# Performance work log

Hardware: AMD Instinct MI355X
Metric: run time of the kernel (lower is better)

## Reference

```python
import jax, jax.numpy as jnp
import numpy as np

N_CLUSTERS = 512
TEMPERATURE = 0.1


def setup_inputs() -> dict:
    key = jax.random.key(0)
    k1, k2 = jax.random.split(key)
    x = jax.random.normal(k1, (32, 1024, 256), dtype=jnp.float32)
    centroids = jax.random.normal(k2, (N_CLUSTERS, 256), dtype=jnp.float32)
    return {"x": x, "centroids": centroids}


def reference(x, centroids):
    # Flatten non-cluster axes into a sample axis: [N, D]
    B, S, D = x.shape
    xf = x.reshape(-1, D)  # [N, D]
    x_sq = jnp.sum(xf * xf, axis=-1, keepdims=True)           # [N, 1]
    c_sq = jnp.sum(centroids * centroids, axis=-1)             # [K]
    cross = jnp.einsum('nd,kd->nk', xf, centroids)             # [N, K]
    dists = x_sq - 2.0 * cross + c_sq[None, :]                 # [N, K]
    # Temperature-scaled soft assignments
    assignments = jax.nn.softmax(-dists / TEMPERATURE, axis=-1)  # [N, K]
    # Restore leading (non-feature) dims, append cluster axis
    return assignments.reshape(B, S, N_CLUSTERS)
```

## Files before the change

### kernel.cpp

```cpp
#include <hip/hip_runtime.h>

#define NROWS 32768
#define KC 512
#define DDIM 256
#define BM 128
#define BK 32
#define KCH (DDIM / BK)
#define CHUNK_USH (KC * BK)

typedef __attribute__((ext_vector_type(8))) short bf16x8;
typedef __attribute__((ext_vector_type(4))) float f32x4;

union U8 { unsigned short u[8]; bf16x8 v; };

__device__ __forceinline__ unsigned short f2bf(float f) {
    union { float f; unsigned int u; } a; a.f = f;
    unsigned int r = a.u + 0x7fffu + ((a.u >> 16) & 1u);
    return (unsigned short)(r >> 16);
}
__device__ __forceinline__ float bf2f(unsigned short h) {
    union { unsigned int u; float f; } a; a.u = ((unsigned int)h) << 16;
    return a.f;
}
__device__ __forceinline__ void ld16(const void* g, void* l) {
    __builtin_amdgcn_global_load_lds(
        (const __attribute__((address_space(1))) unsigned int*)g,
        (__attribute__((address_space(3))) unsigned int*)l, 16, 0, 0);
}

__global__ __launch_bounds__(64) void prep_c(const float* __restrict__ c,
                                             unsigned short* __restrict__ bhi,
                                             unsigned short* __restrict__ blo,
                                             float* __restrict__ csq10) {
    const int n = blockIdx.x, lane = threadIdx.x;
    const int d0 = lane * 4;
    float4 v = ((const float4*)(c + (size_t)n * DDIM))[lane];
    float vv[4] = {v.x, v.y, v.z, v.w};
    unsigned short hh[4], ll[4];
    float ssq = 0.f;
    #pragma unroll
    for (int i = 0; i < 4; ++i) {
        ssq += vv[i] * vv[i];
        hh[i] = f2bf(vv[i]);
        ll[i] = f2bf(vv[i] - bf2f(hh[i]));
    }
    #pragma unroll
    for (int off = 32; off; off >>= 1) ssq += __shfl_xor(ssq, off);
    if (lane == 0) csq10[n] = 10.f * ssq;
    const int ks = d0 >> 5;
    const int q  = (d0 >> 3) & 3;
    const int s  = q ^ ((n >> 1) & 3);
    const size_t dst = (size_t)ks * CHUNK_USH + (n * 4 + s) * 8 + (d0 & 7);
    *(ushort4*)(bhi + dst) = make_ushort4(hh[0], hh[1], hh[2], hh[3]);
    *(ushort4*)(blo + dst) = make_ushort4(ll[0], ll[1], ll[2], ll[3]);
}

union SmemU {
    struct { unsigned short Bh[2][CHUNK_USH], Bl[2][CHUNK_USH]; } k;
    float lbuf[32 * 516];
};

__global__ __launch_bounds__(512, 2) void kmeans_mfma(
    const float* __restrict__ x, const unsigned short* __restrict__ bhi,
    const unsigned short* __restrict__ blo, const float* __restrict__ csq10,
    float* __restrict__ out) {
    __shared__ __align__(16) SmemU sm;
    __shared__ float red[2][2][BM];

    const int tid  = threadIdx.x;
    const int w    = tid >> 6, lane = tid & 63;
    const int wm   = w >> 1, wn = w & 1;
    const int cc   = lane & 15, q = lane >> 4;
    const int row0 = blockIdx.x * BM;

    f32x4 acc[2][16];
    #pragma unroll
    for (int mt = 0; mt < 2; ++mt)
        #pragma unroll
        for (int t = 0; t < 16; ++t) acc[mt][t] = (f32x4){0.f, 0.f, 0.f, 0.f};

    const float* xA0 = x + (size_t)(row0 + wm * 32 + cc) * DDIM + q * 8;
    const float* xA1 = xA0 + (size_t)16 * DDIM;
    const int sF = q ^ ((cc >> 1) & 3);
    const int bF = (4 * cc + sF) * 8;
    const int dmaOff = (w * 4) * 512;

    #pragma unroll
    for (int j = 0; j < 4; ++j) {
        const int o = dmaOff + j * 512;
        ld16(bhi + o + lane * 8, &sm.k.Bh[0][o]);
        ld16(blo + o + lane * 8, &sm.k.Bl[0][o]);
    }
    float4 c00 = *(const float4*)xA0;
    float4 c01 = *(const float4*)(xA0 + 4);
    float4 c10 = *(const float4*)xA1;
    float4 c11 = *(const float4*)(xA1 + 4);
    __syncthreads();

    for (int ks = 0; ks < KCH; ++ks) {
        const int pp = ks & 1;
        float4 n00, n01, n10, n11;
        if (ks < KCH - 1) {
            const size_t cb = (size_t)(ks + 1) * CHUNK_USH;
            #pragma unroll
            for (int j = 0; j < 4; ++j) {
                const int o = dmaOff + j * 512;
                ld16(bhi + cb + o + lane * 8, &sm.k.Bh[1 - pp][o]);
                ld16(blo + cb + o + lane * 8, &sm.k.Bl[1 - pp][o]);
            }
            const int kn = (ks + 1) * BK;
            n00 = *(const float4*)(xA0 + kn);
            n01 = *(const float4*)(xA0 + kn + 4);
            n10 = *(const float4*)(xA1 + kn);
            n11 = *(const float4*)(xA1 + kn + 4);
        }
        bf16x8 ah[2], al[2];
        {
            float v0[8] = {c00.x, c00.y, c00.z, c00.w, c01.x, c01.y, c01.z, c01.w};
            float v1[8] = {c10.x, c10.y, c10.z, c10.w, c11.x, c11.y, c11.z, c11.w};
            U8 H0, L0, H1, L1;
            #pragma unroll
            for (int i = 0; i < 8; ++i) {
                H0.u[i] = f2bf(v0[i]); L0.u[i] = f2bf(v0[i] - bf2f(H0.u[i]));
                H1.u[i] = f2bf(v1[i]); L1.u[i] = f2bf(v1[i] - bf2f(H1.u[i]));
            }
            ah[0] = H0.v; al[0] = L0.v; ah[1] = H1.v; al[1] = L1.v;
        }
        #pragma unroll
        for (int t = 0; t < 16; ++t) {
            const int bo = (wn * 16 + t) * 512 + bF;
            bf16x8 bh = *(const bf16x8*)&sm.k.Bh[pp][bo];
            bf16x8 bl = *(const bf16x8*)&sm.k.Bl[pp][bo];
            acc[0][t] = __builtin_amdgcn_mfma_f32_16x16x32_bf16(ah[0], bh, acc[0][t], 0, 0, 0);
            acc[1][t] = __builtin_amdgcn_mfma_f32_16x16x32_bf16(ah[1], bh, acc[1][t], 0, 0, 0);
            acc[0][t] = __builtin_amdgcn_mfma_f32_16x16x32_bf16(ah[0], bl, acc[0][t], 0, 0, 0);
            acc[1][t] = __builtin_amdgcn_mfma_f32_16x16x32_bf16(ah[1], bl, acc[1][t], 0, 0, 0);
            acc[0][t] = __builtin_amdgcn_mfma_f32_16x16x32_bf16(al[0], bh, acc[0][t], 0, 0, 0);
            acc[1][t] = __builtin_amdgcn_mfma_f32_16x16x32_bf16(al[1], bh, acc[1][t], 0, 0, 0);
        }
        c00 = n00; c01 = n01; c10 = n10; c11 = n11;
        __syncthreads();
    }

    float csqv[16];
    #pragma unroll
    for (int t = 0; t < 16; ++t) csqv[t] = csq10[wn * 256 + t * 16 + cc];
    const int rb = wm * 32 + q * 4;
    float M[2][4], I[2][4];
    #pragma unroll
    for (int mt = 0; mt < 2; ++mt)
        #pragma unroll
        for (int g = 0; g < 4; ++g) {
            float pm = -1e30f;
            #pragma unroll
            for (int t = 0; t < 16; ++t) pm = fmaxf(pm, 20.f * acc[mt][t][g] - csqv[t]);
            #pragma unroll
            for (int off = 1; off < 16; off <<= 1) pm = fmaxf(pm, __shfl_xor(pm, off));
            if (cc == 0) red[0][wn][rb + mt * 16 + g] = pm;
            M[mt][g] = pm;
        }
    __syncthreads();
    #pragma unroll
    for (int mt = 0; mt < 2; ++mt)
        #pragma unroll
        for (int g = 0; g < 4; ++g) {
            M[mt][g] = fmaxf(M[mt][g], red[0][1 - wn][rb + mt * 16 + g]);
            float ps = 0.f;
            #pragma unroll
            for (int t = 0; t < 16; ++t) ps += __expf(20.f * acc[mt][t][g] - csqv[t] - M[mt][g]);
            #pragma unroll
            for (int off = 1; off < 16; off <<= 1) ps += __shfl_xor(ps, off);
            if (cc == 0) red[1][wn][rb + mt * 16 + g] = ps;
        }
    __syncthreads();
    #pragma unroll
    for (int mt = 0; mt < 2; ++mt)
        #pragma unroll
        for (int g = 0; g < 4; ++g)
            I[mt][g] = 1.f / (red[1][0][rb + mt * 16 + g] + red[1][1][rb + mt * 16 + g]);

    #pragma unroll
    for (int p = 0; p < 4; ++p) {
        if (wm == p) {
            #pragma unroll
            for (int mt = 0; mt < 2; ++mt)
                #pragma unroll
                for (int g = 0; g < 4; ++g) {
                    const int   lr = mt * 16 + q * 4 + g;
                    const float mg = M[mt][g], ig = I[mt][g];
                    #pragma unroll
                    for (int t = 0; t < 16; ++t)
                        sm.lbuf[lr * 516 + wn * 256 + t * 16 + cc] =
                            __expf(20.f * acc[mt][t][g] - csqv[t] - mg) * ig;
                }
        }
        __syncthreads();
        #pragma unroll
        for (int j = 0; j < 8; ++j) {
            const int f    = j * 512 + tid;
            const int lrow = f >> 7;
            const int c4   = f & 127;
            float4    v    = *(const float4*)&sm.lbuf[lrow * 516 + c4 * 4];
            *(float4*)(out + (size_t)(row0 + p * 32 + lrow) * KC + c4 * 4) = v;
        }
        __syncthreads();
    }
}

extern "C" void kernel_launch(void* const* d_in, const int* in_sizes, int n_in,
                              void* d_out, int out_size, void* d_ws, size_t ws_size,
                              hipStream_t stream) {
    const float* x   = (const float*)d_in[0];
    const float* c   = (const float*)d_in[1];
    float*       out = (float*)d_out;

    unsigned short* bhi   = (unsigned short*)d_ws;
    unsigned short* blo   = bhi + (size_t)KCH * CHUNK_USH;
    float*          csq10 = (float*)(blo + (size_t)KCH * CHUNK_USH);

    prep_c<<<KC, 64, 0, stream>>>(c, bhi, blo, csq10);
    kmeans_mfma<<<NROWS / BM, 512, 0, stream>>>(x, bhi, blo, csq10, out);
}
```

Before: 118.0 us.

## Halve row tile, single-buffer centroid smem, raise occupancy, stagger K start

Shrinks the row tile from 128 to 64 with a 2x4 warp grid, so each warp keeps 8 instead of 16 accumulator tiles. The centroid chunks move from double buffering to a single buffer, and launch bounds rise to 4 blocks per CU. This trades the overlap of loads with MFMA for more resident blocks and doubles the grid. Blocks also start at a staggered K-chunk offset, which is meant to spread L2 accesses to the centroid data, and the softmax reductions now combine four column warps.

Measured after the change: 122.8 us. 1.04x slower.

```diff
diff --git a/kernel.cpp b/kernel.cpp
--- a/kernel.cpp
+++ b/kernel.cpp
@@ -3,7 +3,7 @@
 #define NROWS 32768
 #define KC 512
 #define DDIM 256
-#define BM 128
+#define BM 64
 #define BK 32
 #define KCH (DDIM / BK)
 #define CHUNK_USH (KC * BK)
@@ -56,59 +56,58 @@
 }
 
 union SmemU {
-    struct { unsigned short Bh[2][CHUNK_USH], Bl[2][CHUNK_USH]; } k;
-    float lbuf[32 * 516];
+    struct { unsigned short Bh[CHUNK_USH], Bl[CHUNK_USH]; } k;
+    float lbuf[16 * 516];
 };
 
-__global__ __launch_bounds__(512, 2) void kmeans_mfma(
+__global__ __launch_bounds__(512, 4) void kmeans_mfma(
     const float* __restrict__ x, const unsigned short* __restrict__ bhi,
     const unsigned short* __restrict__ blo, const float* __restrict__ csq10,
     float* __restrict__ out) {
     __shared__ __align__(16) SmemU sm;
-    __shared__ float red[2][2][BM];
+    __shared__ float red[2][4][BM];
 
     const int tid  = threadIdx.x;
     const int w    = tid >> 6, lane = tid & 63;
-    const int wm   = w >> 1, wn = w & 1;
+    const int wm   = w >> 2, wn = w & 3;
     const int cc   = lane & 15, q = lane >> 4;
     const int row0 = blockIdx.x * BM;
 
-    f32x4 acc[2][16];
-    #pragma unroll
-    for (int mt = 0; mt < 2; ++mt)
-        #pragma unroll
-        for (int t = 0; t < 16; ++t) acc[mt][t] = (f32x4){0.f, 0.f, 0.f, 0.f};
+    f32x4 acc[2][8];
+    #pragma unroll
+    for (int mt = 0; mt < 2; ++mt)
+        #pragma unroll
+        for (int t = 0; t < 8; ++t) acc[mt][t] = (f32x4){0.f, 0.f, 0.f, 0.f};
 
     const float* xA0 = x + (size_t)(row0 + wm * 32 + cc) * DDIM + q * 8;
     const float* xA1 = xA0 + (size_t)16 * DDIM;
     const int sF = q ^ ((cc >> 1) & 3);
     const int bF = (4 * cc + sF) * 8;
-    const int dmaOff = (w * 4) * 512;
-
-    #pragma unroll
-    for (int j = 0; j < 4; ++j) {
-        const int o = dmaOff + j * 512;
-        ld16(bhi + o + lane * 8, &sm.k.Bh[0][o]);
-        ld16(blo + o + lane * 8, &sm.k.Bl[0][o]);
-    }
-    float4 c00 = *(const float4*)xA0;
-    float4 c01 = *(const float4*)(xA0 + 4);
-    float4 c10 = *(const float4*)xA1;
-    float4 c11 = *(const float4*)(xA1 + 4);
+    const int dmaOff = w * 2048;
+
+    const int s0 = ((blockIdx.x >> 3) & 1) * 4;
+
+    {
+        const size_t cb = (size_t)s0 * CHUNK_USH;
+        #pragma unroll
+        for (int j = 0; j < 4; ++j) {
+            const int o = dmaOff + j * 512;
+            ld16(bhi + cb + o + lane * 8, &sm.k.Bh[o]);
+            ld16(blo + cb + o + lane * 8, &sm.k.Bl[o]);
+        }
+    }
+    const int k0 = s0 * BK;
+    float4 c00 = *(const float4*)(xA0 + k0);
+    float4 c01 = *(const float4*)(xA0 + k0 + 4);
+    float4 c10 = *(const float4*)(xA1 + k0);
+    float4 c11 = *(const float4*)(xA1 + k0 + 4);
     __syncthreads();
 
-    for (int ks = 0; ks < KCH; ++ks) {
-        const int pp = ks & 1;
+    for (int i = 0; i < KCH; ++i) {
+        const int nks = (s0 + i + 1) & (KCH - 1);
         float4 n00, n01, n10, n11;
-        if (ks < KCH - 1) {
-            const size_t cb = (size_t)(ks + 1) * CHUNK_USH;
-            #pragma unroll
-            for (int j = 0; j < 4; ++j) {
-                const int o = dmaOff + j * 512;
-                ld16(bhi + cb + o + lane * 8, &sm.k.Bh[1 - pp][o]);
-                ld16(blo + cb + o + lane * 8, &sm.k.Bl[1 - pp][o]);
-            }
-            const int kn = (ks + 1) * BK;
+        if (i < KCH - 1) {
+            const int kn = nks * BK;
             n00 = *(const float4*)(xA0 + kn);
             n01 = *(const float4*)(xA0 + kn + 4);
             n10 = *(const float4*)(xA1 + kn);
@@ -120,17 +119,17 @@
             float v1[8] = {c10.x, c10.y, c10.z, c10.w, c11.x, c11.y, c11.z, c11.w};
             U8 H0, L0, H1, L1;
             #pragma unroll
-            for (int i = 0; i < 8; ++i) {
-                H0.u[i] = f2bf(v0[i]); L0.u[i] = f2bf(v0[i] - bf2f(H0.u[i]));
-                H1.u[i] = f2bf(v1[i]); L1.u[i] = f2bf(v1[i] - bf2f(H1.u[i]));
+            for (int e = 0; e < 8; ++e) {
+                H0.u[e] = f2bf(v0[e]); L0.u[e] = f2bf(v0[e] - bf2f(H0.u[e]));
+                H1.u[e] = f2bf(v1[e]); L1.u[e] = f2bf(v1[e] - bf2f(H1.u[e]));
             }
             ah[0] = H0.v; al[0] = L0.v; ah[1] = H1.v; al[1] = L1.v;
         }
         #pragma unroll
-        for (int t = 0; t < 16; ++t) {
-            const int bo = (wn * 16 + t) * 512 + bF;
-            bf16x8 bh = *(const bf16x8*)&sm.k.Bh[pp][bo];
-            bf16x8 bl = *(const bf16x8*)&sm.k.Bl[pp][bo];
+        for (int t = 0; t < 8; ++t) {
+            const int bo = (wn * 8 + t) * 512 + bF;
+            bf16x8 bh = *(const bf16x8*)&sm.k.Bh[bo];
+            bf16x8 bl = *(const bf16x8*)&sm.k.Bl[bo];
             acc[0][t] = __builtin_amdgcn_mfma_f32_16x16x32_bf16(ah[0], bh, acc[0][t], 0, 0, 0);
             acc[1][t] = __builtin_amdgcn_mfma_f32_16x16x32_bf16(ah[1], bh, acc[1][t], 0, 0, 0);
             acc[0][t] = __builtin_amdgcn_mfma_f32_16x16x32_bf16(ah[0], bl, acc[0][t], 0, 0, 0);
@@ -138,13 +137,23 @@
             acc[0][t] = __builtin_amdgcn_mfma_f32_16x16x32_bf16(al[0], bh, acc[0][t], 0, 0, 0);
             acc[1][t] = __builtin_amdgcn_mfma_f32_16x16x32_bf16(al[1], bh, acc[1][t], 0, 0, 0);
         }
+        __syncthreads();
+        if (i < KCH - 1) {
+            const size_t cb = (size_t)nks * CHUNK_USH;
+            #pragma unroll
+            for (int j = 0; j < 4; ++j) {
+                const int o = dmaOff + j * 512;
+                ld16(bhi + cb + o + lane * 8, &sm.k.Bh[o]);
+                ld16(blo + cb + o + lane * 8, &sm.k.Bl[o]);
+            }
+            __syncthreads();
+        }
         c00 = n00; c01 = n01; c10 = n10; c11 = n11;
-        __syncthreads();
-    }
-
-    float csqv[16];
-    #pragma unroll
-    for (int t = 0; t < 16; ++t) csqv[t] = csq10[wn * 256 + t * 16 + cc];
+    }
+
+    float csqv[8];
+    #pragma unroll
+    for (int t = 0; t < 8; ++t) csqv[t] = csq10[wn * 128 + t * 16 + cc];
     const int rb = wm * 32 + q * 4;
     float M[2][4], I[2][4];
     #pragma unroll
@@ -153,55 +162,59 @@
         for (int g = 0; g < 4; ++g) {
             float pm = -1e30f;
             #pragma unroll
-            for (int t = 0; t < 16; ++t) pm = fmaxf(pm, 20.f * acc[mt][t][g] - csqv[t]);
+            for (int t = 0; t < 8; ++t) pm = fmaxf(pm, 20.f * acc[mt][t][g] - csqv[t]);
             #pragma unroll
             for (int off = 1; off < 16; off <<= 1) pm = fmaxf(pm, __shfl_xor(pm, off));
             if (cc == 0) red[0][wn][rb + mt * 16 + g] = pm;
-            M[mt][g] = pm;
         }
     __syncthreads();
     #pragma unroll
     for (int mt = 0; mt < 2; ++mt)
         #pragma unroll
         for (int g = 0; g < 4; ++g) {
-            M[mt][g] = fmaxf(M[mt][g], red[0][1 - wn][rb + mt * 16 + g]);
+            const int ri = rb + mt * 16 + g;
+            const float m = fmaxf(fmaxf(red[0][0][ri], red[0][1][ri]),
+                                  fmaxf(red[0][2][ri], red[0][3][ri]));
+            M[mt][g] = m;
             float ps = 0.f;
             #pragma unroll
-            for (int t = 0; t < 16; ++t) ps += __expf(20.f * acc[mt][t][g] - csqv[t] - M[mt][g]);
+            for (int t = 0; t < 8; ++t) ps += __expf(20.f * acc[mt][t][g] - csqv[t] - m);
             #pragma unroll
             for (int off = 1; off < 16; off <<= 1) ps += __shfl_xor(ps, off);
-            if (cc == 0) red[1][wn][rb + mt * 16 + g] = ps;
+            if (cc == 0) red[1][wn][ri] = ps;
         }
     __syncthreads();
     #pragma unroll
     for (int mt = 0; mt < 2; ++mt)
         #pragma unroll
-        for (int g = 0; g < 4; ++g)
-            I[mt][g] = 1.f / (red[1][0][rb + mt * 16 + g] + red[1][1][rb + mt * 16 + g]);
+        for (int g = 0; g < 4; ++g) {
+            const int ri = rb + mt * 16 + g;
+            I[mt][g] = 1.f / (red[1][0][ri] + red[1][1][ri] +
+                              red[1][2][ri] + red[1][3][ri]);
+        }
 
     #pragma unroll
     for (int p = 0; p < 4; ++p) {
-        if (wm == p) {
-            #pragma unroll
-            for (int mt = 0; mt < 2; ++mt)
+        if (wm == (p >> 1)) {
+            const int mt = p & 1;
+            #pragma unroll
+            for (int g = 0; g < 4; ++g) {
+                const int   lr = q * 4 + g;
+                const float mg = M[mt][g], ig = I[mt][g];
                 #pragma unroll
-                for (int g = 0; g < 4; ++g) {
-                    const int   lr = mt * 16 + q * 4 + g;
-                    const float mg = M[mt][g], ig = I[mt][g];
-                    #pragma unroll
-                    for (int t = 0; t < 16; ++t)
-                        sm.lbuf[lr * 516 + wn * 256 + t * 16 + cc] =
-                            __expf(20.f * acc[mt][t][g] - csqv[t] - mg) * ig;
-                }
+                for (int t = 0; t < 8; ++t)
+                    sm.lbuf[lr * 516 + wn * 128 + t * 16 + cc] =
+                        __expf(20.f * acc[mt][t][g] - csqv[t] - mg) * ig;
+            }
         }
         __syncthreads();
         #pragma unroll
-        for (int j = 0; j < 8; ++j) {
+        for (int j = 0; j < 4; ++j) {
             const int f    = j * 512 + tid;
             const int lrow = f >> 7;
             const int c4   = f & 127;
             float4    v    = *(const float4*)&sm.lbuf[lrow * 516 + c4 * 4];
-            *(float4*)(out + (size_t)(row0 + p * 32 + lrow) * KC + c4 * 4) = v;
+            *(float4*)(out + (size_t)(row0 + p * 16 + lrow) * KC + c4 * 4) = v;
         }
         __syncthreads();
     }
```

## Load centroid fragments directly from global into registers, drop LDS staging

Applied to the files above, without the earlier changes.

Rewrites prep_c so the bf16 hi/lo centroid fragments are stored in a lane-contiguous MFMA fragment order. The main kernel then loads them straight from global memory into registers, double-buffered two tiles ahead, instead of DMA-staging them through LDS. This removes the LDS ping-pong buffers and the per-chunk __syncthreads, which should also cut LDS use and may help occupancy. In exchange every wave re-reads the centroid data from global/L2, and the MFMAs are exposed to global load latency.

Result: slower. 123.3 us (+4.5%).

```diff
diff --git a/kernel.cpp b/kernel.cpp
--- a/kernel.cpp
+++ b/kernel.cpp
@@ -6,7 +6,6 @@
 #define BM 128
 #define BK 32
 #define KCH (DDIM / BK)
-#define CHUNK_USH (KC * BK)
 
 typedef __attribute__((ext_vector_type(8))) short bf16x8;
 typedef __attribute__((ext_vector_type(4))) float f32x4;
@@ -21,11 +20,6 @@
 __device__ __forceinline__ float bf2f(unsigned short h) {
     union { unsigned int u; float f; } a; a.u = ((unsigned int)h) << 16;
     return a.f;
-}
-__device__ __forceinline__ void ld16(const void* g, void* l) {
-    __builtin_amdgcn_global_load_lds(
-        (const __attribute__((address_space(1))) unsigned int*)g,
-        (__attribute__((address_space(3))) unsigned int*)l, 16, 0, 0);
 }
 
 __global__ __launch_bounds__(64) void prep_c(const float* __restrict__ c,
@@ -49,22 +43,17 @@
     if (lane == 0) csq10[n] = 10.f * ssq;
     const int ks = d0 >> 5;
     const int q  = (d0 >> 3) & 3;
-    const int s  = q ^ ((n >> 1) & 3);
-    const size_t dst = (size_t)ks * CHUNK_USH + (n * 4 + s) * 8 + (d0 & 7);
+    const int t  = n >> 4, cc = n & 15;
+    const size_t dst = ((size_t)(ks * 32 + t) * 64 + (q * 16 + cc)) * 8 + (d0 & 7);
     *(ushort4*)(bhi + dst) = make_ushort4(hh[0], hh[1], hh[2], hh[3]);
     *(ushort4*)(blo + dst) = make_ushort4(ll[0], ll[1], ll[2], ll[3]);
 }
-
-union SmemU {
-    struct { unsigned short Bh[2][CHUNK_USH], Bl[2][CHUNK_USH]; } k;
-    float lbuf[32 * 516];
-};
 
 __global__ __launch_bounds__(512, 2) void kmeans_mfma(
     const float* __restrict__ x, const unsigned short* __restrict__ bhi,
     const unsigned short* __restrict__ blo, const float* __restrict__ csq10,
     float* __restrict__ out) {
-    __shared__ __align__(16) SmemU sm;
+    __shared__ __align__(16) float lbuf[32 * 516];
     __shared__ float red[2][2][BM];
 
     const int tid  = threadIdx.x;
@@ -81,33 +70,15 @@
 
     const float* xA0 = x + (size_t)(row0 + wm * 32 + cc) * DDIM + q * 8;
     const float* xA1 = xA0 + (size_t)16 * DDIM;
-    const int sF = q ^ ((cc >> 1) & 3);
-    const int bF = (4 * cc + sF) * 8;
-    const int dmaOff = (w * 4) * 512;
-
-    #pragma unroll
-    for (int j = 0; j < 4; ++j) {
-        const int o = dmaOff + j * 512;
-        ld16(bhi + o + lane * 8, &sm.k.Bh[0][o]);
-        ld16(blo + o + lane * 8, &sm.k.Bl[0][o]);
-    }
+
     float4 c00 = *(const float4*)xA0;
     float4 c01 = *(const float4*)(xA0 + 4);
     float4 c10 = *(const float4*)xA1;
     float4 c11 = *(const float4*)(xA1 + 4);
-    __syncthreads();
 
     for (int ks = 0; ks < KCH; ++ks) {
-        const int pp = ks & 1;
         float4 n00, n01, n10, n11;
         if (ks < KCH - 1) {
-            const size_t cb = (size_t)(ks + 1) * CHUNK_USH;
-            #pragma unroll
-            for (int j = 0; j < 4; ++j) {
-                const int o = dmaOff + j * 512;
-                ld16(bhi + cb + o + lane * 8, &sm.k.Bh[1 - pp][o]);
-                ld16(blo + cb + o + lane * 8, &sm.k.Bl[1 - pp][o]);
-            }
             const int kn = (ks + 1) * BK;
             n00 = *(const float4*)(xA0 + kn);
             n01 = *(const float4*)(xA0 + kn + 4);
@@ -120,26 +91,42 @@
             float v1[8] = {c10.x, c10.y, c10.z, c10.w, c11.x, c11.y, c11.z, c11.w};
             U8 H0, L0, H1, L1;
             #pragma unroll
-            for (int i = 0; i < 8; ++i) {
-                H0.u[i] = f2bf(v0[i]); L0.u[i] = f2bf(v0[i] - bf2f(H0.u[i]));
-                H1.u[i] = f2bf(v1[i]); L1.u[i] = f2bf(v1[i] - bf2f(H1.u[i]));
+            for (int e = 0; e < 8; ++e) {
+                H0.u[e] = f2bf(v0[e]); L0.u[e] = f2bf(v0[e] - bf2f(H0.u[e]));
+                H1.u[e] = f2bf(v1[e]); L1.u[e] = f2bf(v1[e] - bf2f(H1.u[e]));
             }
             ah[0] = H0.v; al[0] = L0.v; ah[1] = H1.v; al[1] = L1.v;
         }
-        #pragma unroll
-        for (int t = 0; t < 16; ++t) {
-            const int bo = (wn * 16 + t) * 512 + bF;
-            bf16x8 bh = *(const bf16x8*)&sm.k.Bh[pp][bo];
-            bf16x8 bl = *(const bf16x8*)&sm.k.Bl[pp][bo];
-            acc[0][t] = __builtin_amdgcn_mfma_f32_16x16x32_bf16(ah[0], bh, acc[0][t], 0, 0, 0);
-            acc[1][t] = __builtin_amdgcn_mfma_f32_16x16x32_bf16(ah[1], bh, acc[1][t], 0, 0, 0);
-            acc[0][t] = __builtin_amdgcn_mfma_f32_16x16x32_bf16(ah[0], bl, acc[0][t], 0, 0, 0);
-            acc[1][t] = __builtin_amdgcn_mfma_f32_16x16x32_bf16(ah[1], bl, acc[1][t], 0, 0, 0);
-            acc[0][t] = __builtin_amdgcn_mfma_f32_16x16x32_bf16(al[0], bh, acc[0][t], 0, 0, 0);
-            acc[1][t] = __builtin_amdgcn_mfma_f32_16x16x32_bf16(al[1], bh, acc[1][t], 0, 0, 0);
+        const unsigned short* bhp = bhi + ((size_t)(ks * 32 + wn * 16) << 9) + lane * 8;
+        const unsigned short* blp = blo + ((size_t)(ks * 32 + wn * 16) << 9) + lane * 8;
+        bf16x8 pb[2][2][2];
+        pb[0][0][0] = *(const bf16x8*)(bhp);
+        pb[0][0][1] = *(const bf16x8*)(blp);
+        pb[0][1][0] = *(const bf16x8*)(bhp + 512);
+        pb[0][1][1] = *(const bf16x8*)(blp + 512);
+        #pragma unroll
+        for (int tg = 0; tg < 8; ++tg) {
+            const int par = tg & 1, nxt = par ^ 1;
+            if (tg < 7) {
+                pb[nxt][0][0] = *(const bf16x8*)(bhp + (2 * tg + 2) * 512);
+                pb[nxt][0][1] = *(const bf16x8*)(blp + (2 * tg + 2) * 512);
+                pb[nxt][1][0] = *(const bf16x8*)(bhp + (2 * tg + 3) * 512);
+                pb[nxt][1][1] = *(const bf16x8*)(blp + (2 * tg + 3) * 512);
+            }
+            #pragma unroll
+            for (int tt = 0; tt < 2; ++tt) {
+                const int t = 2 * tg + tt;
+                bf16x8 bh = pb[par][tt][0];
+                bf16x8 bl = pb[par][tt][1];
+                acc[0][t] = __builtin_amdgcn_mfma_f32_16x16x32_bf16(ah[0], bh, acc[0][t], 0, 0, 0);
+                acc[1][t] = __builtin_amdgcn_mfma_f32_16x16x32_bf16(ah[1], bh, acc[1][t], 0, 0, 0);
+                acc[0][t] = __builtin_amdgcn_mfma_f32_16x16x32_bf16(ah[0], bl, acc[0][t], 0, 0, 0);
+                acc[1][t] = __builtin_amdgcn_mfma_f32_16x16x32_bf16(ah[1], bl, acc[1][t], 0, 0, 0);
+                acc[0][t] = __builtin_amdgcn_mfma_f32_16x16x32_bf16(al[0], bh, acc[0][t], 0, 0, 0);
+                acc[1][t] = __builtin_amdgcn_mfma_f32_16x16x32_bf16(al[1], bh, acc[1][t], 0, 0, 0);
+            }
         }
         c00 = n00; c01 = n01; c10 = n10; c11 = n11;
-        __syncthreads();
     }
 
     float csqv[16];
@@ -190,7 +177,7 @@
                     const float mg = M[mt][g], ig = I[mt][g];
                     #pragma unroll
                     for (int t = 0; t < 16; ++t)
-                        sm.lbuf[lr * 516 + wn * 256 + t * 16 + cc] =
+                        lbuf[lr * 516 + wn * 256 + t * 16 + cc] =
                             __expf(20.f * acc[mt][t][g] - csqv[t] - mg) * ig;
                 }
         }
@@ -200,7 +187,7 @@
             const int f    = j * 512 + tid;
             const int lrow = f >> 7;
             const int c4   = f & 127;
-            float4    v    = *(const float4*)&sm.lbuf[lrow * 516 + c4 * 4];
+            float4    v    = *(const float4*)&lbuf[lrow * 516 + c4 * 4];
             *(float4*)(out + (size_t)(row0 + p * 32 + lrow) * KC + c4 * 4) = v;
         }
         __syncthreads();
@@ -215,8 +202,8 @@
     float*       out = (float*)d_out;
 
     unsigned short* bhi   = (unsigned short*)d_ws;
-    unsigned short* blo   = bhi + (size_t)KCH * CHUNK_USH;
-    float*          csq10 = (float*)(blo + (size_t)KCH * CHUNK_USH);
+    unsigned short* blo   = bhi + (size_t)KCH * KC * BK;
+    float*          csq10 = (float*)(blo + (size_t)KCH * KC * BK);
 
     prep_c<<<KC, 64, 0, stream>>>(c, bhi, blo, csq10);
     kmeans_mfma<<<NROWS / BM, 512, 0, stream>>>(x, bhi, blo, csq10, out);
```
